# Kernel tuning notes

Measured on AMD Instinct MI355X. Metric: run time of the kernel, lower is better.

Reference implementation:

```python
import jax, jax.numpy as jnp
import numpy as np

TAU = 2.0   # membrane time constant
V_TH = 0.5  # firing threshold

@jax.custom_vjp
def spike_fn(v):
    return jnp.where(v > 0, 1.0, 0.0)

def _spike_fwd(v):
    return spike_fn(v), v

def _spike_bwd(v, g):
    # atan surrogate gradient (alpha=2): d s / d v = 1 / (1 + (pi*v)^2)
    sg = 1.0 / (1.0 + (jnp.pi * v) ** 2)
    return (g * sg,)

spike_fn.defvjp(_spike_fwd, _spike_bwd)


def setup_inputs() -> dict:
    key = jax.random.key(0)
    # [batch, neurons, time] -- time on axis 2, matching moveaxis(x, 2, 0)
    x = jax.random.normal(key, (32, 16384, 100), dtype=jnp.float32)
    return {"x": x}


def reference(x):
    x_seq = jnp.moveaxis(x, 2, 0)  # [T, B, N]
    decay = 1.0 - 1.0 / TAU

    def scan_fn(v, x_t):
        v = v * decay + x_t            # leaky integrate
        s = spike_fn(v - V_TH)         # fire
        v = v - s * V_TH               # soft reset
        return v, s

    v_init = jnp.zeros_like(x_seq[0])
    _, spikes = jax.lax.scan(scan_fn, v_init, x_seq)
    return jnp.moveaxis(spikes, 0, 2)  # [B, N, T]
```

## Files before the change

kernel.cpp:

```cpp
#include <hip/hip_runtime.h>


#define T_STEPS 100
#define T_VEC   25
#define ROWS    64
#define HROWS   32
#define SLOTS   26
#define DECAY   0.5f
#define VTH     0.5f

__device__ __forceinline__ int swz(int c4, int row) {
    return (c4 < 24) ? (c4 ^ (row & 7)) : c4;
}

__global__ __launch_bounds__(64, 3) void lif_kernel(const float* __restrict__ x,
                                                    float* __restrict__ out,
                                                    int n_rows) {
    __shared__ float4 tile[HROWS * SLOTS];

    const int tid = threadIdx.x;
    const long long row0 = (long long)blockIdx.x * ROWS;
    const long long total_f4 = (long long)n_rows * T_VEC;
    const long long gf0 = row0 * T_VEC;

    const float4* __restrict__ xb = reinterpret_cast<const float4*>(x);
    float4* __restrict__ ob       = reinterpret_cast<float4*>(out);

    float4 buf[T_VEC];

    #pragma unroll
    for (int stage = 0; stage < 2; ++stage) {
        const long long gbase = gf0 + (long long)stage * (HROWS * T_VEC);
        #pragma unroll
        for (int k = 0; k < 13; ++k) {
            int f = k * ROWS + tid;
            if (f < HROWS * T_VEC && gbase + f < total_f4) {
                float4 w = xb[gbase + f];
                int r  = f / T_VEC;
                int c4 = f % T_VEC;
                tile[r * SLOTS + swz(c4, r)] = w;
            }
        }
        __syncthreads();
        if ((tid >> 5) == stage) {
            const int r = tid & (HROWS - 1);
            #pragma unroll
            for (int j = 0; j < T_VEC; ++j)
                buf[j] = tile[r * SLOTS + swz(j, r)];
        }
        __syncthreads();
    }

    {
        float v = 0.0f;
        #pragma unroll
        for (int j = 0; j < T_VEC; ++j) {
            float xs[4] = {buf[j].x, buf[j].y, buf[j].z, buf[j].w};
            float ss[4];
            #pragma unroll
            for (int k = 0; k < 4; ++k) {
                v = v * DECAY + xs[k];
                float sk = (v - VTH > 0.0f) ? 1.0f : 0.0f;
                v -= sk * VTH;
                ss[k] = sk;
            }
            buf[j].x = ss[0]; buf[j].y = ss[1]; buf[j].z = ss[2]; buf[j].w = ss[3];
        }
    }

    #pragma unroll
    for (int stage = 0; stage < 2; ++stage) {
        if ((tid >> 5) == stage) {
            const int r = tid & (HROWS - 1);
            #pragma unroll
            for (int j = 0; j < T_VEC; ++j)
                tile[r * SLOTS + swz(j, r)] = buf[j];
        }
        __syncthreads();
        const long long gbase = gf0 + (long long)stage * (HROWS * T_VEC);
        #pragma unroll
        for (int k = 0; k < 13; ++k) {
            int f = k * ROWS + tid;
            if (f < HROWS * T_VEC && gbase + f < total_f4) {
                int r  = f / T_VEC;
                int c4 = f % T_VEC;
                ob[gbase + f] = tile[r * SLOTS + swz(c4, r)];
            }
        }
        __syncthreads();
    }
}

extern "C" void kernel_launch(void* const* d_in, const int* in_sizes, int n_in,
                              void* d_out, int out_size, void* d_ws, size_t ws_size,
                              hipStream_t stream) {
    const float* x = (const float*)d_in[0];
    float* out = (float*)d_out;

    int n_rows = in_sizes[0] / T_STEPS;
    int grid = (n_rows + ROWS - 1) / ROWS;

    lif_kernel<<<grid, ROWS, 0, stream>>>(x, out, n_rows);
}
```

Measured before the change: 97.56 us.

## Use per-wave LDS tiles in 256-thread blocks, drop barriers, nontemporal stores

Each block now holds four independent waves, and each wave owns its own LDS transpose tile. Because a tile is touched by only one wavefront, all __syncthreads barriers are removed. Output stores use nontemporal hints to reduce cache pollution, and the compute step is guarded for tail rows. The risk is that the barrier-free design relies on intra-wave ordering of LDS accesses, and the larger LDS use per block may limit occupancy.

```diff
diff --git a/kernel.cpp b/kernel.cpp
--- a/kernel.cpp
+++ b/kernel.cpp
@@ -3,55 +3,58 @@
 
 #define T_STEPS 100
 #define T_VEC   25
-#define ROWS    64
+#define WROWS   64
 #define HROWS   32
 #define SLOTS   26
+#define WAVES   4
 #define DECAY   0.5f
 #define VTH     0.5f
+
+typedef float vfloat4 __attribute__((ext_vector_type(4)));
 
 __device__ __forceinline__ int swz(int c4, int row) {
     return (c4 < 24) ? (c4 ^ (row & 7)) : c4;
 }
 
-__global__ __launch_bounds__(64, 3) void lif_kernel(const float* __restrict__ x,
-                                                    float* __restrict__ out,
-                                                    int n_rows) {
-    __shared__ float4 tile[HROWS * SLOTS];
+__global__ __launch_bounds__(256, 3) void lif_kernel(const float* __restrict__ x,
+                                                     float* __restrict__ out,
+                                                     int n_rows) {
+    __shared__ vfloat4 tile[WAVES][HROWS * SLOTS];
 
-    const int tid = threadIdx.x;
-    const long long row0 = (long long)blockIdx.x * ROWS;
+    const int lane = threadIdx.x & 63;
+    const int wv   = threadIdx.x >> 6;
+    const long long wid   = (long long)blockIdx.x * WAVES + wv;
+    const long long row0  = wid * WROWS;
     const long long total_f4 = (long long)n_rows * T_VEC;
-    const long long gf0 = row0 * T_VEC;
 
-    const float4* __restrict__ xb = reinterpret_cast<const float4*>(x);
-    float4* __restrict__ ob       = reinterpret_cast<float4*>(out);
+    vfloat4* tw = tile[wv];
+    const vfloat4* __restrict__ xb = reinterpret_cast<const vfloat4*>(x);
+    vfloat4* __restrict__ ob       = reinterpret_cast<vfloat4*>(out);
 
-    float4 buf[T_VEC];
+    vfloat4 buf[T_VEC];
 
     #pragma unroll
     for (int stage = 0; stage < 2; ++stage) {
-        const long long gbase = gf0 + (long long)stage * (HROWS * T_VEC);
+        const long long gbase = (row0 + stage * HROWS) * T_VEC;
         #pragma unroll
         for (int k = 0; k < 13; ++k) {
-            int f = k * ROWS + tid;
+            int f = k * 64 + lane;
             if (f < HROWS * T_VEC && gbase + f < total_f4) {
-                float4 w = xb[gbase + f];
+                vfloat4 w = xb[gbase + f];
                 int r  = f / T_VEC;
                 int c4 = f % T_VEC;
-                tile[r * SLOTS + swz(c4, r)] = w;
+                tw[r * SLOTS + swz(c4, r)] = w;
             }
         }
-        __syncthreads();
-        if ((tid >> 5) == stage) {
-            const int r = tid & (HROWS - 1);
+        if ((lane >> 5) == stage) {
+            const int r = lane & (HROWS - 1);
             #pragma unroll
             for (int j = 0; j < T_VEC; ++j)
-                buf[j] = tile[r * SLOTS + swz(j, r)];
+                buf[j] = tw[r * SLOTS + swz(j, r)];
         }
-        __syncthreads();
     }
 
-    {
+    if (row0 + lane < n_rows) {
         float v = 0.0f;
         #pragma unroll
         for (int j = 0; j < T_VEC; ++j) {
@@ -70,24 +73,23 @@
 
     #pragma unroll
     for (int stage = 0; stage < 2; ++stage) {
-        if ((tid >> 5) == stage) {
-            const int r = tid & (HROWS - 1);
+        if ((lane >> 5) == stage) {
+            const int r = lane & (HROWS - 1);
             #pragma unroll
             for (int j = 0; j < T_VEC; ++j)
-                tile[r * SLOTS + swz(j, r)] = buf[j];
+                tw[r * SLOTS + swz(j, r)] = buf[j];
         }
-        __syncthreads();
-        const long long gbase = gf0 + (long long)stage * (HROWS * T_VEC);
+        const long long gbase = (row0 + stage * HROWS) * T_VEC;
         #pragma unroll
         for (int k = 0; k < 13; ++k) {
-            int f = k * ROWS + tid;
+            int f = k * 64 + lane;
             if (f < HROWS * T_VEC && gbase + f < total_f4) {
                 int r  = f / T_VEC;
                 int c4 = f % T_VEC;
-                ob[gbase + f] = tile[r * SLOTS + swz(c4, r)];
+                vfloat4 w = tw[r * SLOTS + swz(c4, r)];
+                __builtin_nontemporal_store(w, &ob[gbase + f]);
             }
         }
-        __syncthreads();
     }
 }
 
@@ -98,7 +100,8 @@
     float* out = (float*)d_out;
 
     int n_rows = in_sizes[0] / T_STEPS;
-    int grid = (n_rows + ROWS - 1) / ROWS;
+    int rows_per_block = WROWS * WAVES;
+    int grid = (n_rows + rows_per_block - 1) / rows_per_block;
 
-    lif_kernel<<<grid, ROWS, 0, stream>>>(x, out, n_rows);
+    lif_kernel<<<grid, 256, 0, stream>>>(x, out, n_rows);
 }
```

Result: slower. 255.1 us (+161.5%).
